# Performance work log

Measured on AMD Instinct MI355X. Metric: run time of the kernel, lower is better.

## Reference

```python
import jax, jax.numpy as jnp
import numpy as np

N = 50000      # nodes per graph (= num hyperedges, forced by the stack ops)
E = 800000     # incidence pairs per graph
L = 16         # max nodes per hyperedge (padded with index 0)
F_IN = 128     # in_channels
D1 = 256       # dim_1
D2 = D1 // 4   # conv2 out dim = FusionAttention in_size
H_ATT = 128    # FusionAttention hidden_size
EPS = 1e-15


def setup_inputs() -> dict:
    key = jax.random.key(0)
    ks = jax.random.split(key, 32)
    inp = {}
    for i in range(4):
        inp[f"x{i}"] = jax.random.normal(ks[i], (N, F_IN), jnp.float32)
        nidx = jax.random.randint(ks[4 + i], (E,), 0, N, dtype=jnp.int32)
        eidx = jax.random.randint(ks[8 + i], (E,), 0, N, dtype=jnp.int32)
        inp[f"ei{i}"] = jnp.stack([nidx, eidx])  # [2, E]
        hn = jax.random.randint(ks[12 + i], (N, L), 0, N + 1, dtype=jnp.int32)
        inp[f"hnode{i}"] = hn
        # hye_len = number of real (non-padding) entries per hyperedge
        inp[f"hlen{i}"] = jnp.sum(hn > 0, axis=1, keepdims=True).astype(jnp.float32)
    # shared Hgnn params (PyG HypergraphConv: lin without bias + separate bias)
    inp["W1"] = jax.random.normal(ks[16], (F_IN, D1), jnp.float32) / np.sqrt(F_IN).astype(np.float32)
    inp["b1"] = jnp.zeros((D1,), jnp.float32)
    inp["W2"] = jax.random.normal(ks[17], (D1, D2), jnp.float32) / np.sqrt(D1).astype(np.float32)
    inp["b2"] = jnp.zeros((D2,), jnp.float32)
    # two FusionAttention heads: Linear(D2,H_ATT)+Tanh, Linear(H_ATT,1,bias=False)
    for name, a, b in [("ac", 18, 19), ("am", 20, 21)]:
        inp[f"{name}_W1"] = jax.random.normal(ks[a], (D2, H_ATT), jnp.float32) / np.sqrt(D2).astype(np.float32)
        inp[f"{name}_b1"] = jnp.zeros((H_ATT,), jnp.float32)
        inp[f"{name}_W2"] = jax.random.normal(ks[b], (H_ATT, 1), jnp.float32) / np.sqrt(H_ATT).astype(np.float32)
    return inp


def _hconv(x, node_idx, edge_idx, W, b):
    """PyG HypergraphConv (heads=1, unit hyperedge weights):
    X' = D^-1 H B^-1 H^T (X W) + b, via two segment-sum passes."""
    x = x @ W  # [N, out]
    ones = jnp.ones(node_idx.shape, x.dtype)
    deg_n = jax.ops.segment_sum(ones, node_idx, num_segments=N)
    d_inv = jnp.where(deg_n > 0, 1.0 / deg_n, 0.0)
    deg_e = jax.ops.segment_sum(ones, edge_idx, num_segments=N)
    b_inv = jnp.where(deg_e > 0, 1.0 / deg_e, 0.0)
    # node -> hyperedge: m_e = B^-1[e] * sum_{v in e} x[v]
    efeat = b_inv[:, None] * jax.ops.segment_sum(x[node_idx], edge_idx, num_segments=N)
    # hyperedge -> node: out_v = D^-1[v] * sum_{e : v in e} m_e
    out = d_inv[:, None] * jax.ops.segment_sum(efeat[edge_idx], node_idx, num_segments=N)
    return out + b


def _hgnn(x, ei, W1, b1, W2, b2):
    x = jax.nn.relu(_hconv(x, ei[0], ei[1], W1, b1))
    return jax.nn.relu(_hconv(x, ei[0], ei[1], W2, b2))


def _hye_emb(node_emb, hlen, hnode):
    # prepend zero row so padding index 0 gathers zeros
    padded = jnp.concatenate([jnp.zeros((1, node_emb.shape[1]), node_emb.dtype), node_emb], axis=0)
    seq = padded[hnode]                    # [M, L, F]
    return jnp.sum(seq, axis=1) / (hlen + EPS)


def _fusion_attn(z, W1, b1, W2):
    # z: [N, 4, d]
    w = (jnp.tanh(z @ W1 + b1) @ W2).mean(0)      # [4, 1]
    beta = jax.nn.softmax(w, axis=0)              # [4, 1]
    return jnp.sum(beta * z, axis=1)              # [N, d]


def reference(x0, x1, x2, x3, ei0, ei1, ei2, ei3,
              hlen0, hlen1, hlen2, hlen3, hnode0, hnode1, hnode2, hnode3,
              W1, b1, W2, b2, ac_W1, ac_b1, ac_W2, am_W1, am_b1, am_W2):
    x1_cm = _hgnn(x0, ei0, W1, b1, W2, b2)
    x1_mc = _hgnn(x1, ei1, W1, b1, W2, b2)
    x1_cc = _hgnn(x2, ei2, W1, b1, W2, b2)
    x1_mm = _hgnn(x3, ei3, W1, b1, W2, b2)
    x2_cm = _hye_emb(x1_cm, hlen0, hnode0)
    x2_mc = _hye_emb(x1_mc, hlen1, hnode1)
    x2_cc = _hye_emb(x1_cc, hlen2, hnode2)
    x2_mm = _hye_emb(x1_mm, hlen3, hnode3)
    x_c = jnp.stack((x1_mc, x2_cm, x1_cc, x2_cc), axis=1)  # [N, 4, D2]
    x_m = jnp.stack((x1_cm, x2_mc, x1_mm, x2_mm), axis=1)
    h_c = _fusion_attn(x_c, ac_W1, ac_b1, ac_W2)
    h_m = _fusion_attn(x_m, am_W1, am_b1, am_W2)
    return (h_c, h_m)
```

## Files before the change

kernel.cpp:

```cpp
#include <hip/hip_runtime.h>
#include <hip/hip_bf16.h>

#define NF   128
#define DD1  256
#define DD2  64
#define HATT 128

static inline int cdiv(int a, int b) { return (a + b - 1) / b; }

__global__ __launch_bounds__(256) void count_rank(const int* __restrict__ nidx,
                                                  const int* __restrict__ eidx,
                                                  int* __restrict__ deg,
                                                  int* __restrict__ rank,
                                                  int N, int E) {
    int e = blockIdx.x * 256 + threadIdx.x;
    if (e < E) {
        const int vn = nidx[e], ve = eidx[e];
        const int rn = atomicAdd(&deg[vn], 1);
        const int re = atomicAdd(&deg[N + ve], 1);
        rank[e] = rn | (re << 16);
    }
}

__global__ __launch_bounds__(256) void scan_blocks(const int* __restrict__ in,
// ... 106 lines not shown
        a.rank[(size_t)g * a.E + e] = rn | (re << 16);
    }
}

__global__ __launch_bounds__(256) void build_fill_b(BuildB a) {
    const int g = blockIdx.y;
    const int shard = blockIdx.x & 7;
    const int chunk = blockIdx.x >> 3;
    const int lo = shard * a.shardSize;
    const int hi = lo + a.shardSize;
    const int base = chunk * 1024;
    const int* __restrict__ nidx = a.nidx[g];
    const int* __restrict__ eidx = a.eidx[g];
    const int* __restrict__ rank = a.rank + (size_t)g * a.E;
    const int* __restrict__ off  = a.off + (size_t)g * 2 * a.Nn;
#pragma unroll
    for (int i = 0; i < 4; i++) {
        const int e = base + i * 256 + threadIdx.x;
        if (e < a.E) {
            const int vn = nidx[e], ve = eidx[e];
            const int rk = rank[e];
            if (vn >= lo && vn < hi)
                a.srcidx[off[vn] + (rk & 0xffff)] = ve;
            if (ve >= lo && ve < hi)
                a.srcidx[off[a.Nn + ve] + (rk >> 16)] = vn;
        }
    }
}

__global__ __launch_bounds__(256) void gather_rows_128(const float* __restrict__ src,
                                                       const int* __restrict__ off,
                                                       const int* __restrict__ srcidx,
                                                       const float* __restrict__ scale,
                                                       float* __restrict__ dst, int Nn) {
    const int row = blockIdx.x * 16 + (threadIdx.x >> 4);
    if (row >= Nn) return;
    const int c = (threadIdx.x & 15) << 2;
    const int j0 = off[row], j1 = off[row + 1];
    float4 pa = make_float4(0.f, 0.f, 0.f, 0.f);
    float4 pb = make_float4(0.f, 0.f, 0.f, 0.f);
    float4 qa = make_float4(0.f, 0.f, 0.f, 0.f);
    float4 qb = make_float4(0.f, 0.f, 0.f, 0.f);
    int j = j0;
    for (; j + 3 < j1; j += 4) {
        const int s0 = srcidx[j + 0];
        const int s1 = srcidx[j + 1];
        const int s2 = srcidx[j + 2];
        const int s3 = srcidx[j + 3];
        const float4 v0a = *(const float4*)&src[(size_t)s0 * 128 + c];
        const float4 v0b = *(const float4*)&src[(size_t)s0 * 128 + c + 64];
        const float4 v1a = *(const float4*)&src[(size_t)s1 * 128 + c];
        const float4 v1b = *(const float4*)&src[(size_t)s1 * 128 + c + 64];
        const float4 v2a = *(const float4*)&src[(size_t)s2 * 128 + c];
        const float4 v2b = *(const float4*)&src[(size_t)s2 * 128 + c + 64];
        const float4 v3a = *(const float4*)&src[(size_t)s3 * 128 + c];
        const float4 v3b = *(const float4*)&src[(size_t)s3 * 128 + c + 64];
        pa.x += v0a.x + v1a.x; pa.y += v0a.y + v1a.y;
        pa.z += v0a.z + v1a.z; pa.w += v0a.w + v1a.w;
        qa.x += v2a.x + v3a.x; qa.y += v2a.y + v3a.y;
        qa.z += v2a.z + v3a.z; qa.w += v2a.w + v3a.w;
        pb.x += v0b.x + v1b.x; pb.y += v0b.y + v1b.y;
        pb.z += v0b.z + v1b.z; pb.w += v0b.w + v1b.w;
        qb.x += v2b.x + v3b.x; qb.y += v2b.y + v3b.y;
        qb.z += v2b.z + v3b.z; qb.w += v2b.w + v3b.w;
    }
    for (; j < j1; j++) {
        const int s0 = srcidx[j];
        const float4 va = *(const float4*)&src[(size_t)s0 * 128 + c];
        const float4 vb = *(const float4*)&src[(size_t)s0 * 128 + c + 64];
        pa.x += va.x; pa.y += va.y; pa.z += va.z; pa.w += va.w;
        pb.x += vb.x; pb.y += vb.y; pb.z += vb.z; pb.w += vb.w;
    }
    float4 aca = make_float4(pa.x + qa.x, pa.y + qa.y, pa.z + qa.z, pa.w + qa.w);
    float4 acb = make_float4(pb.x + qb.x, pb.y + qb.y, pb.z + qb.z, pb.w + qb.w);
    if (scale) {
        const float s = scale[row];
        aca.x *= s; aca.y *= s; aca.z *= s; aca.w *= s;
        acb.x *= s; acb.y *= s; acb.z *= s; acb.w *= s;
    }
    *(float4*)&dst[(size_t)row * 128 + c] = aca;
    *(float4*)&dst[(size_t)row * 128 + c + 64] = acb;
}

struct Gather128B {
    const float* src[4];
    float* dst;
    const int* off;
    const int* srcidx;
    const float* dinv;
    int passBase;
    int Nn;
};

__global__ __launch_bounds__(256) void gather128_b(Gather128B a) {
    const int gr = blockIdx.x * 16 + (threadIdx.x >> 4);
    if (gr >= 4 * a.Nn) return;
    const int g = gr / a.Nn;
    const int row = gr - g * a.Nn;
    const float* __restrict__ src = a.src[g];
    const int ob = g * 2 * a.Nn + a.passBase + row;
    const int c = (threadIdx.x & 15) << 2;
    const int j0 = a.off[ob], j1 = a.off[ob + 1];
    float4 pa = make_float4(0.f, 0.f, 0.f, 0.f);
    float4 pb = make_float4(0.f, 0.f, 0.f, 0.f);
    float4 qa = make_float4(0.f, 0.f, 0.f, 0.f);
    float4 qb = make_float4(0.f, 0.f, 0.f, 0.f);
    int j = j0;
    for (; j + 3 < j1; j += 4) {
        const int s0 = a.srcidx[j + 0];
        const int s1 = a.srcidx[j + 1];
        const int s2 = a.srcidx[j + 2];
        const int s3 = a.srcidx[j + 3];
        const float4 v0a = *(const float4*)&src[(size_t)s0 * 128 + c];
        const float4 v0b = *(const float4*)&src[(size_t)s0 * 128 + c + 64];
        const float4 v1a = *(const float4*)&src[(size_t)s1 * 128 + c];
        const float4 v1b = *(const float4*)&src[(size_t)s1 * 128 + c + 64];
        const float4 v2a = *(const float4*)&src[(size_t)s2 * 128 + c];
        const float4 v2b = *(const float4*)&src[(size_t)s2 * 128 + c + 64];
        const float4 v3a = *(const float4*)&src[(size_t)s3 * 128 + c];
        const float4 v3b = *(const float4*)&src[(size_t)s3 * 128 + c + 64];
        pa.x += v0a.x + v1a.x; pa.y += v0a.y + v1a.y;
        pa.z += v0a.z + v1a.z; pa.w += v0a.w + v1a.w;
        qa.x += v2a.x + v3a.x; qa.y += v2a.y + v3a.y;
        qa.z += v2a.z + v3a.z; qa.w += v2a.w + v3a.w;
        pb.x += v0b.x + v1b.x; pb.y += v0b.y + v1b.y;
        pb.z += v0b.z + v1b.z; pb.w += v0b.w + v1b.w;
        qb.x += v2b.x + v3b.x; qb.y += v2b.y + v3b.y;
        qb.z += v2b.z + v3b.z; qb.w += v2b.w + v3b.w;
    }
    for (; j < j1; j++) {
        const int s0 = a.srcidx[j];
        const float4 va = *(const float4*)&src[(size_t)s0 * 128 + c];
        const float4 vb = *(const float4*)&src[(size_t)s0 * 128 + c + 64];
        pa.x += va.x; pa.y += va.y; pa.z += va.z; pa.w += va.w;
        pb.x += vb.x; pb.y += vb.y; pb.z += vb.z; pb.w += vb.w;
    }
    float4 aca = make_float4(pa.x + qa.x, pa.y + qa.y, pa.z + qa.z, pa.w + qa.w);
    float4 acb = make_float4(pb.x + qb.x, pb.y + qb.y, pb.z + qb.z, pb.w + qb.w);
    if (a.dinv) {
        const float s = a.dinv[ob];
        aca.x *= s; aca.y *= s; aca.z *= s; aca.w *= s;
        acb.x *= s; acb.y *= s; acb.z *= s; acb.w *= s;
    }
    *(float4*)&a.dst[(size_t)gr * 128 + c] = aca;
    *(float4*)&a.dst[(size_t)gr * 128 + c + 64] = acb;
}

__global__ __launch_bounds__(256) void gather_rows_64(const float* __restrict__ src,
                                                      const int* __restrict__ off,
                                                      const int* __restrict__ srcidx,
                                                      const float* __restrict__ scale,
                                                      const float* __restrict__ post_bias,
                                                      float* __restrict__ dst, int Nn) {
    const int row = blockIdx.x * 32 + (threadIdx.x >> 3);
    if (row >= Nn) return;
    const int c = (threadIdx.x & 7) << 2;
    const int j0 = off[row], j1 = off[row + 1];
    float4 pa = make_float4(0.f, 0.f, 0.f, 0.f);
    float4 pb = make_float4(0.f, 0.f, 0.f, 0.f);
    float4 qa = make_float4(0.f, 0.f, 0.f, 0.f);
    float4 qb = make_float4(0.f, 0.f, 0.f, 0.f);
    int j = j0;
    for (; j + 3 < j1; j += 4) {
        const int s0 = srcidx[j + 0];
        const int s1 = srcidx[j + 1];
        const int s2 = srcidx[j + 2];
        const int s3 = srcidx[j + 3];
        const float4 v0a = *(const float4*)&src[(size_t)s0 * 64 + c];
        const float4 v0b = *(const float4*)&src[(size_t)s0 * 64 + c + 32];
        const float4 v1a = *(const float4*)&src[(size_t)s1 * 64 + c];
        const float4 v1b = *(const float4*)&src[(size_t)s1 * 64 + c + 32];
        const float4 v2a = *(const float4*)&src[(size_t)s2 * 64 + c];
        const float4 v2b = *(const float4*)&src[(size_t)s2 * 64 + c + 32];
        const float4 v3a = *(const float4*)&src[(size_t)s3 * 64 + c];
        const float4 v3b = *(const float4*)&src[(size_t)s3 * 64 + c + 32];
        pa.x += v0a.x + v1a.x; pa.y += v0a.y + v1a.y;
        pa.z += v0a.z + v1a.z; pa.w += v0a.w + v1a.w;
        qa.x += v2a.x + v3a.x; qa.y += v2a.y + v3a.y;
        qa.z += v2a.z + v3a.z; qa.w += v2a.w + v3a.w;
        pb.x += v0b.x + v1b.x; pb.y += v0b.y + v1b.y;
        pb.z += v0b.z + v1b.z; pb.w += v0b.w + v1b.w;
        qb.x += v2b.x + v3b.x; qb.y += v2b.y + v3b.y;
        qb.z += v2b.z + v3b.z; qb.w += v2b.w + v3b.w;
// ... 91 lines not shown
        aca.x = fmaxf(aca.x + a.post_bias[c + 0], 0.f);
        aca.y = fmaxf(aca.y + a.post_bias[c + 1], 0.f);
        aca.z = fmaxf(aca.z + a.post_bias[c + 2], 0.f);
        aca.w = fmaxf(aca.w + a.post_bias[c + 3], 0.f);
        acb.x = fmaxf(acb.x + a.post_bias[c + 32], 0.f);
        acb.y = fmaxf(acb.y + a.post_bias[c + 33], 0.f);
        acb.z = fmaxf(acb.z + a.post_bias[c + 34], 0.f);
        acb.w = fmaxf(acb.w + a.post_bias[c + 35], 0.f);
    }
    *(float4*)&a.dst[(size_t)gr * 64 + c] = aca;
    *(float4*)&a.dst[(size_t)gr * 64 + c + 32] = acb;
}

__global__ __launch_bounds__(256) void gemm1_f32(const float* __restrict__ A,
                                                 const float* __restrict__ B,
                                                 float* __restrict__ C, int M,
                                                 const float* __restrict__ dinv,
                                                 const float* __restrict__ bias) {
    __shared__ float As[32][132];
    __shared__ float Bs[32][128];
    const int tid = threadIdx.x;
    const int m0 = blockIdx.y * 128;
    const int bn = blockIdx.x * 128;
    const int rq = (tid >> 4) << 2;
    const int cq = (tid & 15) << 2;

    float acc[8][8] = {{0.f}};

    for (int k0 = 0; k0 < 128; k0 += 32) {
#pragma unroll
        for (int i = 0; i < 4; i++) {
            const int f = tid + 256 * i;
            const int r = f >> 3;
            const int q = (f & 7) << 2;
            const int grow = m0 + r;
            float4 v = make_float4(0.f, 0.f, 0.f, 0.f);
            if (grow < M) v = *(const float4*)&A[(size_t)grow * 128 + k0 + q];
            As[q + 0][r] = v.x;
            As[q + 1][r] = v.y;
            As[q + 2][r] = v.z;
            As[q + 3][r] = v.w;
        }
#pragma unroll
        for (int i = 0; i < 4; i++) {
            const int f = tid + 256 * i;
            const int r = f >> 5;
            const int c4 = (f & 31) << 2;
            *(float4*)&Bs[r][c4] = *(const float4*)&B[(size_t)(k0 + r) * 256 + bn + c4];
        }
        __syncthreads();
#pragma unroll
        for (int k = 0; k < 32; k++) {
            float av[8], bv[8];
            *(float4*)&av[0] = *(const float4*)&As[k][rq];
            *(float4*)&av[4] = *(const float4*)&As[k][rq + 64];
            *(float4*)&bv[0] = *(const float4*)&Bs[k][cq];
            *(float4*)&bv[4] = *(const float4*)&Bs[k][cq + 64];
#pragma unroll
            for (int r = 0; r < 8; r++)
#pragma unroll
                for (int c = 0; c < 8; c++)
                    acc[r][c] = fmaf(av[r], bv[c], acc[r][c]);
        }
        __syncthreads();
    }
#pragma unroll
    for (int r = 0; r < 8; r++) {
        const int grow = m0 + rq + (r & 3) + ((r >> 2) << 6);
        if (grow < M) {
            const float s = dinv[grow];
            float o[8];
#pragma unroll
            for (int c = 0; c < 4; c++)
                o[c] = fmaxf(fmaf(acc[r][c], s, bias[bn + cq + c]), 0.f);
#pragma unroll
            for (int c = 4; c < 8; c++)
                o[c] = fmaxf(fmaf(acc[r][c], s, bias[bn + 64 + cq + (c - 4)]), 0.f);
            *(float4*)&C[(size_t)grow * 256 + bn + cq] = *(float4*)&o[0];
            *(float4*)&C[(size_t)grow * 256 + bn + 64 + cq] = *(float4*)&o[4];
        }
    }
}

struct Gemm1B {
    const float* A;
    const float* B;
    float* C[4];
    const float* dinv;
    const float* bias;
    int Nn;
};

__global__ __launch_bounds__(256) void gemm1_b(Gemm1B a) {
    __shared__ float As[32][132];
    __shared__ float Bs[32][128];
    const int M = 4 * a.Nn;
    const int tid = threadIdx.x;
    const int m0 = blockIdx.y * 128;
    const int bn = blockIdx.x * 128;
    const int rq = (tid >> 4) << 2;
    const int cq = (tid & 15) << 2;

    float acc[8][8] = {{0.f}};

    for (int k0 = 0; k0 < 128; k0 += 32) {
#pragma unroll
        for (int i = 0; i < 4; i++) {
            const int f = tid + 256 * i;
            const int r = f >> 3;
            const int q = (f & 7) << 2;
            const int grow = m0 + r;
            float4 v = make_float4(0.f, 0.f, 0.f, 0.f);
            if (grow < M) v = *(const float4*)&a.A[(size_t)grow * 128 + k0 + q];
            As[q + 0][r] = v.x;
            As[q + 1][r] = v.y;
            As[q + 2][r] = v.z;
            As[q + 3][r] = v.w;
        }
#pragma unroll
        for (int i = 0; i < 4; i++) {
            const int f = tid + 256 * i;
            const int r = f >> 5;
            const int c4 = (f & 31) << 2;
            *(float4*)&Bs[r][c4] = *(const float4*)&a.B[(size_t)(k0 + r) * 256 + bn + c4];
        }
        __syncthreads();
#pragma unroll
        for (int k = 0; k < 32; k++) {
            float av[8], bv[8];
            *(float4*)&av[0] = *(const float4*)&As[k][rq];
            *(float4*)&av[4] = *(const float4*)&As[k][rq + 64];
            *(float4*)&bv[0] = *(const float4*)&Bs[k][cq];
            *(float4*)&bv[4] = *(const float4*)&Bs[k][cq + 64];
#pragma unroll
            for (int r = 0; r < 8; r++)
#pragma unroll
                for (int c = 0; c < 8; c++)
                    acc[r][c] = fmaf(av[r], bv[c], acc[r][c]);
        }
        __syncthreads();
    }
#pragma unroll
    for (int r = 0; r < 8; r++) {
        const int grow = m0 + rq + (r & 3) + ((r >> 2) << 6);
        if (grow < M) {
            const int g = grow / a.Nn;
            const int lr = grow - g * a.Nn;
            const float s = a.dinv[(size_t)g * 2 * a.Nn + lr];
            float* Cg = a.C[g] + (size_t)lr * 256;
            float o[8];
#pragma unroll
            for (int c = 0; c < 4; c++)
                o[c] = fmaxf(fmaf(acc[r][c], s, a.bias[bn + cq + c]), 0.f);
#pragma unroll
            for (int c = 4; c < 8; c++)
                o[c] = fmaxf(fmaf(acc[r][c], s, a.bias[bn + 64 + cq + (c - 4)]), 0.f);
            *(float4*)&Cg[bn + cq] = *(float4*)&o[0];
            *(float4*)&Cg[bn + 64 + cq] = *(float4*)&o[4];
        }
    }
}

__global__ __launch_bounds__(256) void gemm2_f32(const float* __restrict__ A,
                                                 const float* __restrict__ B,
                                                 float* __restrict__ C, int M) {
    __shared__ float As[32][132];
    __shared__ float Bs[32][64];
    const int tid = threadIdx.x;
    const int m0 = blockIdx.y * 128;
    const int tr = (tid >> 3) << 2;
    const int tc = (tid & 7) << 3;

    float acc[4][8] = {{0.f}};

    for (int k0 = 0; k0 < 256; k0 += 32) {
#pragma unroll
        for (int i = 0; i < 4; i++) {
            const int f = tid + 256 * i;
            const int r = f >> 3;
            const int q = (f & 7) << 2;
            const int grow = m0 + r;
            float4 v = make_float4(0.f, 0.f, 0.f, 0.f);
            if (grow < M) v = *(const float4*)&A[(size_t)grow * 256 + k0 + q];
            As[q + 0][r] = v.x;
            As[q + 1][r] = v.y;
            As[q + 2][r] = v.z;
            As[q + 3][r] = v.w;
        }
#pragma unroll
        for (int i = 0; i < 2; i++) {
            const int f = tid + 256 * i;
            const int r = f >> 4;
            const int c4 = (f & 15) << 2;
            *(float4*)&Bs[r][c4] = *(const float4*)&B[(size_t)(k0 + r) * 64 + c4];
        }
        __syncthreads();
#pragma unroll
        for (int k = 0; k < 32; k++) {
            float av[4], bv[8];
            *(float4*)&av[0] = *(const float4*)&As[k][tr];
            *(float4*)&bv[0] = *(const float4*)&Bs[k][tc];
            *(float4*)&bv[4] = *(const float4*)&Bs[k][tc + 4];
#pragma unroll
            for (int r = 0; r < 4; r++)
#pragma unroll
                for (int c = 0; c < 8; c++)
                    acc[r][c] = fmaf(av[r], bv[c], acc[r][c]);
        }
        __syncthreads();
    }
#pragma unroll
    for (int r = 0; r < 4; r++) {
        const int grow = m0 + tr + r;
        if (grow < M) {
            *(float4*)&C[(size_t)grow * 64 + tc] =
                make_float4(acc[r][0], acc[r][1], acc[r][2], acc[r][3]);
            *(float4*)&C[(size_t)grow * 64 + tc + 4] =
                make_float4(acc[r][4], acc[r][5], acc[r][6], acc[r][7]);
        }
    }
}

struct Gemm2B {
    const float* A[4];
    const float* B;
    float* C;
    int Nn;
};

__global__ __launch_bounds__(256) void gemm2_b(Gemm2B a) {
    __shared__ float As[32][132];
    __shared__ float Bs[32][64];
    const int M = 4 * a.Nn;
    const int tid = threadIdx.x;
    const int m0 = blockIdx.y * 128;
    const int tr = (tid >> 3) << 2;
    const int tc = (tid & 7) << 3;

    float acc[4][8] = {{0.f}};

    for (int k0 = 0; k0 < 256; k0 += 32) {
#pragma unroll
        for (int i = 0; i < 4; i++) {
            const int f = tid + 256 * i;
            const int r = f >> 3;
            const int q = (f & 7) << 2;
            const int grow = m0 + r;
            float4 v = make_float4(0.f, 0.f, 0.f, 0.f);
            if (grow < M) {
                const int g = grow / a.Nn;
                const int lr = grow - g * a.Nn;
                v = *(const float4*)&a.A[g][(size_t)lr * 256 + k0 + q];
            }
            As[q + 0][r] = v.x;
            As[q + 1][r] = v.y;
            As[q + 2][r] = v.z;
            As[q + 3][r] = v.w;
        }
#pragma unroll
        for (int i = 0; i < 2; i++) {
            const int f = tid + 256 * i;
            const int r = f >> 4;
            const int c4 = (f & 15) << 2;
            *(float4*)&Bs[r][c4] = *(const float4*)&a.B[(size_t)(k0 + r) * 64 + c4];
        }
        __syncthreads();
#pragma unroll
        for (int k = 0; k < 32; k++) {
            float av[4], bv[8];
            *(float4*)&av[0] = *(const float4*)&As[k][tr];
            *(float4*)&bv[0] = *(const float4*)&Bs[k][tc];
            *(float4*)&bv[4] = *(const float4*)&Bs[k][tc + 4];
#pragma unroll
            for (int r = 0; r < 4; r++)
#pragma unroll
                for (int c = 0; c < 8; c++)
                    acc[r][c] = fmaf(av[r], bv[c], acc[r][c]);
        }
        __syncthreads();
    }
#pragma unroll
    for (int r = 0; r < 4; r++) {
        const int grow = m0 + tr + r;
        if (grow < M) {
            *(float4*)&a.C[(size_t)grow * 64 + tc] =
                make_float4(acc[r][0], acc[r][1], acc[r][2], acc[r][3]);
            *(float4*)&a.C[(size_t)grow * 64 + tc + 4] =
                make_float4(acc[r][4], acc[r][5], acc[r][6], acc[r][7]);
        }
    }
}

__global__ __launch_bounds__(256) void hye_emb_kernel(const float* __restrict__ emb,
                                                      const int* __restrict__ hnode,
                                                      const float* __restrict__ hlen,
                                                      float* __restrict__ out, int Nn) {
    const int r = blockIdx.x * 16 + (threadIdx.x >> 4);
    const int c = (threadIdx.x & 15) << 2;
    if (r >= Nn) return;
    const int4* hp4 = (const int4*)&hnode[(size_t)r * 16];
    const int4 w0 = hp4[0], w1 = hp4[1], w2 = hp4[2], w3 = hp4[3];
    int idx[16] = {w0.x, w0.y, w0.z, w0.w, w1.x, w1.y, w1.z, w1.w,
                   w2.x, w2.y, w2.z, w2.w, w3.x, w3.y, w3.z, w3.w};
    float4 a0 = make_float4(0.f, 0.f, 0.f, 0.f);
    float4 a1 = make_float4(0.f, 0.f, 0.f, 0.f);
    float4 a2 = make_float4(0.f, 0.f, 0.f, 0.f);
    float4 a3 = make_float4(0.f, 0.f, 0.f, 0.f);
#pragma unroll
    for (int l = 0; l < 16; l += 4) {
        if (idx[l + 0] > 0) {
            const float4 v = *(const float4*)&emb[(size_t)(idx[l + 0] - 1) * 64 + c];
            a0.x += v.x; a0.y += v.y; a0.z += v.z; a0.w += v.w;
        }
        if (idx[l + 1] > 0) {
            const float4 v = *(const float4*)&emb[(size_t)(idx[l + 1] - 1) * 64 + c];
            a1.x += v.x; a1.y += v.y; a1.z += v.z; a1.w += v.w;
        }
        if (idx[l + 2] > 0) {
            const float4 v = *(const float4*)&emb[(size_t)(idx[l + 2] - 1) * 64 + c];
            a2.x += v.x; a2.y += v.y; a2.z += v.z; a2.w += v.w;
        }
        if (idx[l + 3] > 0) {
            const float4 v = *(const float4*)&emb[(size_t)(idx[l + 3] - 1) * 64 + c];
            a3.x += v.x; a3.y += v.y; a3.z += v.z; a3.w += v.w;
        }
    }
    const float inv = 1.0f / (hlen[r] + 1e-15f);
    float4 acc;
    acc.x = (a0.x + a1.x + a2.x + a3.x) * inv;
    acc.y = (a0.y + a1.y + a2.y + a3.y) * inv;
    acc.z = (a0.z + a1.z + a2.z + a3.z) * inv;
    acc.w = (a0.w + a1.w + a2.w + a3.w) * inv;
    *(float4*)&out[(size_t)r * 64 + c] = acc;
}

struct HyeB {
    const float* emb;
    const int* hnode[4];
    const float* hlen[4];
    float* out;
    int Nn;
};

__global__ __launch_bounds__(256) void hye_b(HyeB a) {
    const int gr = blockIdx.x * 16 + (threadIdx.x >> 4);
    const int c = (threadIdx.x & 15) << 2;
    if (gr >= 4 * a.Nn) return;
    const int g = gr / a.Nn;
    const int lr = gr - g * a.Nn;
    const float* __restrict__ emb = a.emb + (size_t)g * a.Nn * 64;
    const int4* hp4 = (const int4*)&a.hnode[g][(size_t)lr * 16];
    const int4 w0 = hp4[0], w1 = hp4[1], w2 = hp4[2], w3 = hp4[3];
    int idx[16] = {w0.x, w0.y, w0.z, w0.w, w1.x, w1.y, w1.z, w1.w,
                   w2.x, w2.y, w2.z, w2.w, w3.x, w3.y, w3.z, w3.w};
    float4 a0 = make_float4(0.f, 0.f, 0.f, 0.f);
    float4 a1 = make_float4(0.f, 0.f, 0.f, 0.f);
    float4 a2 = make_float4(0.f, 0.f, 0.f, 0.f);
    float4 a3 = make_float4(0.f, 0.f, 0.f, 0.f);
#pragma unroll
    for (int l = 0; l < 16; l += 4) {
        if (idx[l + 0] > 0) {
            const float4 v = *(const float4*)&emb[(size_t)(idx[l + 0] - 1) * 64 + c];
            a0.x += v.x; a0.y += v.y; a0.z += v.z; a0.w += v.w;
        }
        if (idx[l + 1] > 0) {
            const float4 v = *(const float4*)&emb[(size_t)(idx[l + 1] - 1) * 64 + c];
            a1.x += v.x; a1.y += v.y; a1.z += v.z; a1.w += v.w;
        }
        if (idx[l + 2] > 0) {
            const float4 v = *(const float4*)&emb[(size_t)(idx[l + 2] - 1) * 64 + c];
            a2.x += v.x; a2.y += v.y; a2.z += v.z; a2.w += v.w;
        }
// ... 85 lines not shown
        if (m0 + mq + r < a.Nn) {
#pragma unroll
            for (int c = 0; c < 8; c++) {
                float s = acc[r][c] + b1v[c];
                s = fminf(fmaxf(s, -15.f), 15.f);
                const float t = __expf(2.f * s);
                local += (1.f - 2.f / (t + 1.f)) * w2v[c];
            }
        }
    }
#pragma unroll
    for (int off = 32; off >= 1; off >>= 1) local += __shfl_down(local, off, 64);
    if ((tid & 63) == 0) red[tid >> 6] = local;
    __syncthreads();
    if (tid == 0) atomicAdd(&a.accw[gy], red[0] + red[1] + red[2] + red[3]);
}

__global__ void softmax_beta(const float* __restrict__ acc, float* __restrict__ beta,
                             float invN) {
    const int t = threadIdx.x;
    if (t < 2) {
        const float* a = acc + 4 * t;
        float* b = beta + 4 * t;
        float w[4], m = -1e30f;
#pragma unroll
        for (int i = 0; i < 4; i++) { w[i] = a[i] * invN; m = fmaxf(m, w[i]); }
        float s = 0.f;
#pragma unroll
        for (int i = 0; i < 4; i++) { w[i] = expf(w[i] - m); s += w[i]; }
#pragma unroll
        for (int i = 0; i < 4; i++) b[i] = w[i] / s;
    }
}

__global__ __launch_bounds__(256) void weighted_sum(const float* __restrict__ z0,
                                                    const float* __restrict__ z1,
                                                    const float* __restrict__ z2,
                                                    const float* __restrict__ z3,
                                                    const float* __restrict__ beta,
                                                    float* __restrict__ out, int Nn) {
    const int t = blockIdx.x * 256 + threadIdx.x;
    if (t >= Nn * 16) return;
    const float b0 = beta[0], b1 = beta[1], b2 = beta[2], b3 = beta[3];
    const float4 v0 = *(const float4*)&z0[(size_t)t * 4];
    const float4 v1 = *(const float4*)&z1[(size_t)t * 4];
    const float4 v2 = *(const float4*)&z2[(size_t)t * 4];
    const float4 v3 = *(const float4*)&z3[(size_t)t * 4];
    float4 o;
    o.x = b0 * v0.x + b1 * v1.x + b2 * v2.x + b3 * v3.x;
    o.y = b0 * v0.y + b1 * v1.y + b2 * v2.y + b3 * v3.y;
    o.z = b0 * v0.z + b1 * v1.z + b2 * v2.z + b3 * v3.z;
    o.w = b0 * v0.w + b1 * v1.w + b2 * v2.w + b3 * v3.w;
    *(float4*)&out[(size_t)t * 4] = o;
}

extern "C" void kernel_launch(void* const* d_in, const int* in_sizes, int n_in,
                              void* d_out, int out_size, void* d_ws, size_t ws_size,
                              hipStream_t stream) {
    const int Nn = in_sizes[0] / NF;
    const int E  = in_sizes[1] / 2;
    const int N2 = 2 * Nn;

    const float* x[4];
    const int*   ei[4];
    const int*   hnode[4];
    const float* hlen[4];
    for (int g = 0; g < 4; g++) {
        x[g]     = (const float*)d_in[4 * g + 0];
        ei[g]    = (const int*)d_in[4 * g + 1];
        hnode[g] = (const int*)d_in[4 * g + 2];
        hlen[g]  = (const float*)d_in[4 * g + 3];
    }
    const float* W1   = (const float*)d_in[16];
    const float* b1   = (const float*)d_in[17];
    const float* W2   = (const float*)d_in[18];
    const float* b2   = (const float*)d_in[19];
    const float* acW1 = (const float*)d_in[20];
    const float* acb1 = (const float*)d_in[21];
    const float* acW2 = (const float*)d_in[22];
    const float* amW1 = (const float*)d_in[23];
    const float* amb1 = (const float*)d_in[24];
    const float* amW2 = (const float*)d_in[25];

    const size_t fB1   = (size_t)4 * Nn * 128;
    const size_t fB2   = (size_t)4 * Nn * 128;
    const size_t fH2   = (size_t)4 * Nn * 64;
    const size_t fHE   = (size_t)4 * Nn * 64;
    const size_t fDinv = (size_t)4 * N2;
    const size_t fcnt  = fB1 + fB2 + fH2 + fHE + fDinv + 16;
    const size_t icnt  = (size_t)4 * N2 + ((size_t)4 * N2 + 4) + 512 +
                         (size_t)4 * E + (size_t)8 * E;
    const size_t need  = (fcnt + icnt) * sizeof(float) + 1024;

    if (need <= ws_size) {
        float* ws = (float*)d_ws;
        size_t o = 0;
        float* B1    = ws + o; o += fB1;
        float* B2    = ws + o; o += fB2;
        float* h2b   = ws + o; o += fH2;
        float* hembb = ws + o; o += fHE;
        float* dinv  = ws + o; o += fDinv;
        float* accw  = ws + o; o += 8;
        float* beta  = ws + o; o += 8;
        int* iws = (int*)(ws + o);
        size_t io = 0;
        int* deg      = iws + io; io += (size_t)4 * N2;
        int* off      = iws + io; io += (size_t)4 * N2 + 4;
        int* partials = iws + io; io += 512;
        int* rank     = iws + io; io += (size_t)4 * E;
        int* srcidx   = iws + io; io += (size_t)8 * E;

        float* C1p[4] = { B1, B1 + (size_t)Nn * 256, h2b, hembb };
        float* Dbuf = B2;
        float* E1   = B2 + (size_t)Nn * 256;

        const int n8  = 4 * N2;
        const int nScanBlocks = cdiv(n8, 1024);

        BuildB bb;
        for (int g = 0; g < 4; g++) { bb.nidx[g] = ei[g]; bb.eidx[g] = ei[g] + E; }
        bb.deg = deg; bb.rank = rank; bb.off = off; bb.srcidx = srcidx;
        bb.Nn = Nn; bb.E = E; bb.shardSize = cdiv(Nn, 8);

        hipMemsetAsync(deg, 0, (size_t)n8 * sizeof(int), stream);
        count_rank_b<<<dim3(cdiv(E, 256), 4), 256, 0, stream>>>(bb);
        scan_blocks<<<nScanBlocks, 256, 0, stream>>>(deg, off, partials, n8);
        scan_partials<<<1, 512, 0, stream>>>(partials, nScanBlocks);
        scan_add<<<cdiv(n8, 256), 256, 0, stream>>>(off, partials, n8, 2 * 4 * E);
        build_fill_b<<<dim3(8 * cdiv(E, 1024), 4), 256, 0, stream>>>(bb);
        invert_deg_int<<<cdiv(n8, 256), 256, 0, stream>>>(deg, dinv, n8);

        Gather128B g1;
        for (int g = 0; g < 4; g++) g1.src[g] = x[g];
        g1.dst = B1; g1.off = off; g1.srcidx = srcidx;
        g1.dinv = dinv; g1.passBase = Nn; g1.Nn = Nn;
        gather128_b<<<cdiv(4 * Nn, 16), 256, 0, stream>>>(g1);

        Gather128B g2;
        for (int g = 0; g < 4; g++) g2.src[g] = B1 + (size_t)g * Nn * 128;
        g2.dst = B2; g2.off = off; g2.srcidx = srcidx;
        g2.dinv = nullptr; g2.passBase = 0; g2.Nn = Nn;
        gather128_b<<<cdiv(4 * Nn, 16), 256, 0, stream>>>(g2);

        Gemm1B gm1;
        gm1.A = B2; gm1.B = W1;
        for (int g = 0; g < 4; g++) gm1.C[g] = C1p[g];
        gm1.dinv = dinv; gm1.bias = b1; gm1.Nn = Nn;
        gemm1_b<<<dim3(2, cdiv(4 * Nn, 128)), 256, 0, stream>>>(gm1);

        Gemm2B gm2;
        for (int g = 0; g < 4; g++) gm2.A[g] = C1p[g];
        gm2.B = W2; gm2.C = Dbuf; gm2.Nn = Nn;
        gemm2_b<<<dim3(1, cdiv(4 * Nn, 128)), 256, 0, stream>>>(gm2);

        Gather64B g3;
        for (int g = 0; g < 4; g++) g3.src[g] = Dbuf + (size_t)g * Nn * 64;
        g3.dst = E1; g3.off = off; g3.srcidx = srcidx;
        g3.dinv = dinv; g3.post_bias = nullptr; g3.passBase = Nn; g3.Nn = Nn;
        gather64_b<<<cdiv(4 * Nn, 32), 256, 0, stream>>>(g3);

        Gather64B g4;
        for (int g = 0; g < 4; g++) g4.src[g] = E1 + (size_t)g * Nn * 64;
        g4.dst = h2b; g4.off = off; g4.srcidx = srcidx;
        g4.dinv = dinv; g4.post_bias = b2; g4.passBase = 0; g4.Nn = Nn;
        gather64_b<<<cdiv(4 * Nn, 32), 256, 0, stream>>>(g4);

        HyeB hb;
        hb.emb = h2b;
        for (int g = 0; g < 4; g++) { hb.hnode[g] = hnode[g]; hb.hlen[g] = hlen[g]; }
        hb.out = hembb; hb.Nn = Nn;
        hye_b<<<cdiv(4 * Nn, 16), 256, 0, stream>>>(hb);

        const size_t st = (size_t)Nn * 64;
        hipMemsetAsync(accw, 0, 8 * sizeof(float), stream);
        AttnArgs aa;
        aa.z[0] = h2b + 1 * st; aa.z[1] = hembb + 0 * st;
        aa.z[2] = h2b + 2 * st; aa.z[3] = hembb + 2 * st;
        aa.z[4] = h2b + 0 * st; aa.z[5] = hembb + 1 * st;
        aa.z[6] = h2b + 3 * st; aa.z[7] = hembb + 3 * st;
        aa.W1c = acW1; aa.b1c = acb1; aa.W2c = acW2;
        aa.W1m = amW1; aa.b1m = amb1; aa.W2m = amW2;
        aa.accw = accw; aa.Nn = Nn;
        attn_gemm<<<dim3(cdiv(Nn, 64), 8), 256, 0, stream>>>(aa);
        softmax_beta<<<1, 64, 0, stream>>>(accw, beta, 1.0f / (float)Nn);

        float* out = (float*)d_out;
        weighted_sum<<<cdiv(Nn * 16, 256), 256, 0, stream>>>(
            aa.z[0], aa.z[1], aa.z[2], aa.z[3], beta + 0, out, Nn);
        weighted_sum<<<cdiv(Nn * 16, 256), 256, 0, stream>>>(
            aa.z[4], aa.z[5], aa.z[6], aa.z[7], beta + 4, out + (size_t)Nn * DD2, Nn);
        return;
    }

    float* ws = (float*)d_ws;
    size_t o = 0;
    float* bufA = ws + o; o += (size_t)Nn * DD1;
    float* bufB = ws + o; o += (size_t)Nn * DD1;
    float* dinv = ws + o; o += N2;
    float* h2[4];
    float* hemb[4];
    for (int g = 0; g < 4; g++) { h2[g]   = ws + o; o += (size_t)Nn * DD2; }
    for (int g = 0; g < 4; g++) { hemb[g] = ws + o; o += (size_t)Nn * DD2; }
    float* accw = ws + o; o += 8;
    float* beta = ws + o; o += 8;
    int* iws = (int*)(ws + o);
    size_t io = 0;
    int* deg_i    = iws + io; io += N2;
    int* off      = iws + io; io += N2 + 1;
    int* partials = iws + io; io += 512;
    int* rank     = iws + io; io += E;
    int* srcidx   = iws + io; io += (size_t)2 * E;

    const int nScanBlocks = cdiv(N2, 1024);
    const int shardSize = cdiv(Nn, 8);

    for (int g = 0; g < 4; g++) {
        const int* nidx = ei[g];
        const int* eidx = ei[g] + E;
        const int* off_n = off;
        const int* off_e = off + Nn;
        const float* d_inv = dinv;
        const float* b_inv = dinv + Nn;

        hipMemsetAsync(deg_i, 0, (size_t)N2 * sizeof(int), stream);
        count_rank<<<cdiv(E, 256), 256, 0, stream>>>(nidx, eidx, deg_i, rank, Nn, E);
        scan_blocks<<<nScanBlocks, 256, 0, stream>>>(deg_i, off, partials, N2);
        scan_partials<<<1, 512, 0, stream>>>(partials, nScanBlocks);
        scan_add<<<cdiv(N2, 256), 256, 0, stream>>>(off, partials, N2, 2 * E);
        build_fill<<<8 * cdiv(E, 1024), 256, 0, stream>>>(nidx, eidx, rank, off,
                                                          srcidx, Nn, E, shardSize);
        invert_deg_int<<<cdiv(N2, 256), 256, 0, stream>>>(deg_i, dinv, N2);

        gather_rows_128<<<cdiv(Nn, 16), 256, 0, stream>>>(x[g], off_e, srcidx, b_inv, bufB, Nn);
        gather_rows_128<<<cdiv(Nn, 16), 256, 0, stream>>>(bufB, off_n, srcidx, nullptr, bufA, Nn);
        gemm1_f32<<<dim3(2, cdiv(Nn, 128)), 256, 0, stream>>>(bufA, W1, bufB, Nn, d_inv, b1);

        gemm2_f32<<<dim3(1, cdiv(Nn, 128)), 256, 0, stream>>>(bufB, W2, bufA, Nn);
        gather_rows_64<<<cdiv(Nn, 32), 256, 0, stream>>>(bufA, off_e, srcidx, b_inv,
                                                         nullptr, bufB, Nn);
        gather_rows_64<<<cdiv(Nn, 32), 256, 0, stream>>>(bufB, off_n, srcidx, d_inv,
                                                         b2, h2[g], Nn);

        hye_emb_kernel<<<cdiv(Nn, 16), 256, 0, stream>>>(h2[g], hnode[g], hlen[g], hemb[g], Nn);
    }

    hipMemsetAsync(accw, 0, 8 * sizeof(float), stream);
    AttnArgs aa;
    aa.z[0] = h2[1]; aa.z[1] = hemb[0]; aa.z[2] = h2[2]; aa.z[3] = hemb[2];
    aa.z[4] = h2[0]; aa.z[5] = hemb[1]; aa.z[6] = h2[3]; aa.z[7] = hemb[3];
// ... 13 lines not shown
```

Measured before the change: 1.875 ms.

## Fuse two hypergraph GEMMs into one kernel and shrink workspace via buffer aliasing

Merges the 128->256 and 256->64 GEMMs into one kernel that keeps the 256-wide intermediate in shared memory, so that intermediate never goes to global memory. The 128-wide gathers now run in two halves of two graphs each, and deg/rank/intermediate buffers are aliased onto one region to cut the workspace footprint and improve cache residency. The fused GEMM uses small 32-row tiles with a scalar second-stage inner loop, which may lower compute efficiency. The split gathers add kernel launches.

```diff
diff --git a/kernel.cpp b/kernel.cpp
--- a/kernel.cpp
+++ b/kernel.cpp
@@ -212,23 +212,24 @@
     *(float4*)&dst[(size_t)row * 128 + c + 64] = acb;
 }
 
-struct Gather128B {
-    const float* src[4];
+struct Gather128H {
+    const float* src[2];
     float* dst;
     const int* off;
     const int* srcidx;
     const float* dinv;
+    int gbase;
     int passBase;
     int Nn;
 };
 
-__global__ __launch_bounds__(256) void gather128_b(Gather128B a) {
+__global__ __launch_bounds__(256) void gather128_h(Gather128H a) {
     const int gr = blockIdx.x * 16 + (threadIdx.x >> 4);
-    if (gr >= 4 * a.Nn) return;
-    const int g = gr / a.Nn;
-    const int row = gr - g * a.Nn;
-    const float* __restrict__ src = a.src[g];
-    const int ob = g * 2 * a.Nn + a.passBase + row;
+    if (gr >= 2 * a.Nn) return;
+    const int gl = gr / a.Nn;
+    const int row = gr - gl * a.Nn;
+    const float* __restrict__ src = a.src[gl];
+    const int ob = (a.gbase + gl) * 2 * a.Nn + a.passBase + row;
     const int c = (threadIdx.x & 15) << 2;
     const int j0 = a.off[ob], j1 = a.off[ob + 1];
     float4 pa = make_float4(0.f, 0.f, 0.f, 0.f);
@@ -486,85 +487,6 @@
     }
 }
 
-struct Gemm1B {
-    const float* A;
-    const float* B;
-    float* C[4];
-    const float* dinv;
-    const float* bias;
-    int Nn;
-};
-
-__global__ __launch_bounds__(256) void gemm1_b(Gemm1B a) {
-    __shared__ float As[32][132];
-    __shared__ float Bs[32][128];
-    const int M = 4 * a.Nn;
-    const int tid = threadIdx.x;
-    const int m0 = blockIdx.y * 128;
-    const int bn = blockIdx.x * 128;
-    const int rq = (tid >> 4) << 2;
-    const int cq = (tid & 15) << 2;
-
-    float acc[8][8] = {{0.f}};
-
-    for (int k0 = 0; k0 < 128; k0 += 32) {
-#pragma unroll
-        for (int i = 0; i < 4; i++) {
-            const int f = tid + 256 * i;
-            const int r = f >> 3;
-            const int q = (f & 7) << 2;
-            const int grow = m0 + r;
-            float4 v = make_float4(0.f, 0.f, 0.f, 0.f);
-            if (grow < M) v = *(const float4*)&a.A[(size_t)grow * 128 + k0 + q];
-            As[q + 0][r] = v.x;
-            As[q + 1][r] = v.y;
-            As[q + 2][r] = v.z;
-            As[q + 3][r] = v.w;
-        }
-#pragma unroll
-        for (int i = 0; i < 4; i++) {
-            const int f = tid + 256 * i;
-            const int r = f >> 5;
-            const int c4 = (f & 31) << 2;
-            *(float4*)&Bs[r][c4] = *(const float4*)&a.B[(size_t)(k0 + r) * 256 + bn + c4];
-        }
-        __syncthreads();
-#pragma unroll
-        for (int k = 0; k < 32; k++) {
-            float av[8], bv[8];
-            *(float4*)&av[0] = *(const float4*)&As[k][rq];
-            *(float4*)&av[4] = *(const float4*)&As[k][rq + 64];
-            *(float4*)&bv[0] = *(const float4*)&Bs[k][cq];
-            *(float4*)&bv[4] = *(const float4*)&Bs[k][cq + 64];
-#pragma unroll
-            for (int r = 0; r < 8; r++)
-#pragma unroll
-                for (int c = 0; c < 8; c++)
-                    acc[r][c] = fmaf(av[r], bv[c], acc[r][c]);
-        }
-        __syncthreads();
-    }
-#pragma unroll
-    for (int r = 0; r < 8; r++) {
-        const int grow = m0 + rq + (r & 3) + ((r >> 2) << 6);
-        if (grow < M) {
-            const int g = grow / a.Nn;
-            const int lr = grow - g * a.Nn;
-            const float s = a.dinv[(size_t)g * 2 * a.Nn + lr];
-            float* Cg = a.C[g] + (size_t)lr * 256;
-            float o[8];
-#pragma unroll
-            for (int c = 0; c < 4; c++)
-                o[c] = fmaxf(fmaf(acc[r][c], s, a.bias[bn + cq + c]), 0.f);
-#pragma unroll
-            for (int c = 4; c < 8; c++)
-                o[c] = fmaxf(fmaf(acc[r][c], s, a.bias[bn + 64 + cq + (c - 4)]), 0.f);
-            *(float4*)&Cg[bn + cq] = *(float4*)&o[0];
-            *(float4*)&Cg[bn + 64 + cq] = *(float4*)&o[4];
-        }
-    }
-}
-
 __global__ __launch_bounds__(256) void gemm2_f32(const float* __restrict__ A,
                                                  const float* __restrict__ B,
                                                  float* __restrict__ C, int M) {
@@ -625,56 +547,59 @@
     }
 }
 
-struct Gemm2B {
-    const float* A[4];
-    const float* B;
-    float* C;
+struct Gemm12B {
+    const float* A;
+    const float* W1;
+    const float* W2;
+    const float* b1;
+    const float* dinv;
+    float* D;
     int Nn;
 };
 
-__global__ __launch_bounds__(256) void gemm2_b(Gemm2B a) {
-    __shared__ float As[32][132];
-    __shared__ float Bs[32][64];
-    const int M = 4 * a.Nn;
+#define TS_LD 33
+
+__global__ __launch_bounds__(256) void gemm12_b(Gemm12B a) {
+    __shared__ float smem[9472];
+    float* As  = smem;
+    float* Bs  = smem + 1152;
+    float* Ts  = smem;
+    float* W2s = smem + 8448;
+
+    const int M4 = 4 * a.Nn;
     const int tid = threadIdx.x;
-    const int m0 = blockIdx.y * 128;
-    const int tr = (tid >> 3) << 2;
-    const int tc = (tid & 7) << 3;
+    const int m0 = blockIdx.x * 32;
+    const int rq = (tid >> 5) << 2;
+    const int cq = (tid & 31) << 2;
 
     float acc[4][8] = {{0.f}};
 
-    for (int k0 = 0; k0 < 256; k0 += 32) {
-#pragma unroll
-        for (int i = 0; i < 4; i++) {
-            const int f = tid + 256 * i;
-            const int r = f >> 3;
-            const int q = (f & 7) << 2;
+    for (int k0 = 0; k0 < 128; k0 += 32) {
+        {
+            const int r = tid >> 3;
+            const int q = (tid & 7) << 2;
             const int grow = m0 + r;
             float4 v = make_float4(0.f, 0.f, 0.f, 0.f);
-            if (grow < M) {
-                const int g = grow / a.Nn;
-                const int lr = grow - g * a.Nn;
-                v = *(const float4*)&a.A[g][(size_t)lr * 256 + k0 + q];
-            }
-            As[q + 0][r] = v.x;
-            As[q + 1][r] = v.y;
-            As[q + 2][r] = v.z;
-            As[q + 3][r] = v.w;
-        }
-#pragma unroll
-        for (int i = 0; i < 2; i++) {
+            if (grow < M4) v = *(const float4*)&a.A[(size_t)grow * 128 + k0 + q];
+            As[(q + 0) * 36 + r] = v.x;
+            As[(q + 1) * 36 + r] = v.y;
+            As[(q + 2) * 36 + r] = v.z;
+            As[(q + 3) * 36 + r] = v.w;
+        }
+#pragma unroll
+        for (int i = 0; i < 8; i++) {
             const int f = tid + 256 * i;
-            const int r = f >> 4;
-            const int c4 = (f & 15) << 2;
-            *(float4*)&Bs[r][c4] = *(const float4*)&a.B[(size_t)(k0 + r) * 64 + c4];
+            const int r = f >> 6;
+            const int c4 = (f & 63) << 2;
+            *(float4*)&Bs[r * 256 + c4] = *(const float4*)&a.W1[(size_t)(k0 + r) * 256 + c4];
         }
         __syncthreads();
 #pragma unroll
         for (int k = 0; k < 32; k++) {
             float av[4], bv[8];
-            *(float4*)&av[0] = *(const float4*)&As[k][tr];
-            *(float4*)&bv[0] = *(const float4*)&Bs[k][tc];
-            *(float4*)&bv[4] = *(const float4*)&Bs[k][tc + 4];
+            *(float4*)&av[0] = *(const float4*)&As[k * 36 + rq];
+            *(float4*)&bv[0] = *(const float4*)&Bs[k * 256 + cq];
+            *(float4*)&bv[4] = *(const float4*)&Bs[k * 256 + cq + 128];
 #pragma unroll
             for (int r = 0; r < 4; r++)
 #pragma unroll
@@ -683,15 +608,64 @@
         }
         __syncthreads();
     }
+
+    {
+        float b1lo[4], b1hi[4], s[4];
+#pragma unroll
+        for (int j = 0; j < 4; j++) {
+            b1lo[j] = a.b1[cq + j];
+            b1hi[j] = a.b1[cq + 128 + j];
+        }
+#pragma unroll
+        for (int r = 0; r < 4; r++) {
+            const int gr = m0 + rq + r;
+            float sv = 0.f;
+            if (gr < M4) {
+                const int g = gr / a.Nn;
+                const int lr = gr - g * a.Nn;
+                sv = a.dinv[(size_t)g * 2 * a.Nn + lr];
+            }
+            s[r] = sv;
+        }
+#pragma unroll
+        for (int r = 0; r < 4; r++)
+#pragma unroll
+            for (int j = 0; j < 4; j++) {
+                Ts[(cq + j) * TS_LD + rq + r] =
+                    fmaxf(fmaf(acc[r][j], s[r], b1lo[j]), 0.f);
+                Ts[(cq + 128 + j) * TS_LD + rq + r] =
+                    fmaxf(fmaf(acc[r][4 + j], s[r], b1hi[j]), 0.f);
+            }
+    }
+
+    const int c2 = (tid & 31) << 1;
+    float d0[4] = {0.f, 0.f, 0.f, 0.f};
+    float d1[4] = {0.f, 0.f, 0.f, 0.f};
+    for (int kk = 0; kk < 256; kk += 16) {
+        __syncthreads();
+        {
+            const int r = tid >> 4;
+            const int c4 = (tid & 15) << 2;
+            *(float4*)&W2s[r * 64 + c4] = *(const float4*)&a.W2[(size_t)(kk + r) * 64 + c4];
+        }
+        __syncthreads();
+#pragma unroll
+        for (int k = 0; k < 16; k++) {
+            const float* tr = &Ts[(kk + k) * TS_LD + rq];
+            const float t0 = tr[0], t1 = tr[1], t2 = tr[2], t3 = tr[3];
+            const float w0 = W2s[k * 64 + c2];
+            const float w1 = W2s[k * 64 + c2 + 1];
+            d0[0] = fmaf(t0, w0, d0[0]); d1[0] = fmaf(t0, w1, d1[0]);
+            d0[1] = fmaf(t1, w0, d0[1]); d1[1] = fmaf(t1, w1, d1[1]);
+            d0[2] = fmaf(t2, w0, d0[2]); d1[2] = fmaf(t2, w1, d1[2]);
+            d0[3] = fmaf(t3, w0, d0[3]); d1[3] = fmaf(t3, w1, d1[3]);
+        }
+    }
 #pragma unroll
     for (int r = 0; r < 4; r++) {
-        const int grow = m0 + tr + r;
-        if (grow < M) {
-            *(float4*)&a.C[(size_t)grow * 64 + tc] =
-                make_float4(acc[r][0], acc[r][1], acc[r][2], acc[r][3]);
-            *(float4*)&a.C[(size_t)grow * 64 + tc + 4] =
-                make_float4(acc[r][4], acc[r][5], acc[r][6], acc[r][7]);
-        }
+        const int gr = m0 + rq + r;
+        if (gr < M4)
+            *(float2*)&a.D[(size_t)gr * 64 + c2] = make_float2(d0[r], d1[r]);
     }
 }
 
@@ -943,39 +917,32 @@
     const float* amb1 = (const float*)d_in[24];
     const float* amW2 = (const float*)d_in[25];
 
-    const size_t fB1   = (size_t)4 * Nn * 128;
-    const size_t fB2   = (size_t)4 * Nn * 128;
-    const size_t fH2   = (size_t)4 * Nn * 64;
-    const size_t fHE   = (size_t)4 * Nn * 64;
+    const size_t fRA   = (size_t)4 * Nn * 64;
+    const size_t fRB   = (size_t)4 * Nn * 128;
     const size_t fDinv = (size_t)4 * N2;
-    const size_t fcnt  = fB1 + fB2 + fH2 + fHE + fDinv + 16;
-    const size_t icnt  = (size_t)4 * N2 + ((size_t)4 * N2 + 4) + 512 +
-                         (size_t)4 * E + (size_t)8 * E;
-    const size_t need  = (fcnt + icnt) * sizeof(float) + 1024;
-
-    if (need <= ws_size) {
+    const size_t fcnt  = fRA + fRB + fDinv + 16;
+    const size_t icnt  = ((size_t)4 * N2 + 4) + 512 + (size_t)8 * E;
+    const size_t need  = (fcnt + icnt) * sizeof(float) + 256;
+    const bool raFitsInts = fRA * sizeof(float) >=
+                            ((size_t)4 * N2 + (size_t)4 * E) * sizeof(int);
+
+    if (need <= ws_size && raFitsInts) {
         float* ws = (float*)d_ws;
         size_t o = 0;
-        float* B1    = ws + o; o += fB1;
-        float* B2    = ws + o; o += fB2;
-        float* h2b   = ws + o; o += fH2;
-        float* hembb = ws + o; o += fHE;
-        float* dinv  = ws + o; o += fDinv;
-        float* accw  = ws + o; o += 8;
-        float* beta  = ws + o; o += 8;
+        float* RA   = ws + o; o += fRA;
+        float* RB   = ws + o; o += fRB;
+        float* dinv = ws + o; o += fDinv;
+        float* accw = ws + o; o += 8;
+        float* beta = ws + o; o += 8;
         int* iws = (int*)(ws + o);
         size_t io = 0;
-        int* deg      = iws + io; io += (size_t)4 * N2;
         int* off      = iws + io; io += (size_t)4 * N2 + 4;
         int* partials = iws + io; io += 512;
-        int* rank     = iws + io; io += (size_t)4 * E;
         int* srcidx   = iws + io; io += (size_t)8 * E;
-
-        float* C1p[4] = { B1, B1 + (size_t)Nn * 256, h2b, hembb };
-        float* Dbuf = B2;
-        float* E1   = B2 + (size_t)Nn * 256;
-
-        const int n8  = 4 * N2;
+        int* deg  = (int*)RA;
+        int* rank = deg + (size_t)4 * N2;
+
+        const int n8 = 4 * N2;
         const int nScanBlocks = cdiv(n8, 1024);
 
         BuildB bb;
@@ -991,29 +958,31 @@
         build_fill_b<<<dim3(8 * cdiv(E, 1024), 4), 256, 0, stream>>>(bb);
         invert_deg_int<<<cdiv(n8, 256), 256, 0, stream>>>(deg, dinv, n8);
 
-        Gather128B g1;
-        for (int g = 0; g < 4; g++) g1.src[g] = x[g];
-        g1.dst = B1; g1.off = off; g1.srcidx = srcidx;
-        g1.dinv = dinv; g1.passBase = Nn; g1.Nn = Nn;
-        gather128_b<<<cdiv(4 * Nn, 16), 256, 0, stream>>>(g1);
-
-        Gather128B g2;
-        for (int g = 0; g < 4; g++) g2.src[g] = B1 + (size_t)g * Nn * 128;
-        g2.dst = B2; g2.off = off; g2.srcidx = srcidx;
-        g2.dinv = nullptr; g2.passBase = 0; g2.Nn = Nn;
-        gather128_b<<<cdiv(4 * Nn, 16), 256, 0, stream>>>(g2);
-
-        Gemm1B gm1;
-        gm1.A = B2; gm1.B = W1;
-        for (int g = 0; g < 4; g++) gm1.C[g] = C1p[g];
-        gm1.dinv = dinv; gm1.bias = b1; gm1.Nn = Nn;
-        gemm1_b<<<dim3(2, cdiv(4 * Nn, 128)), 256, 0, stream>>>(gm1);
-
-        Gemm2B gm2;
-        for (int g = 0; g < 4; g++) gm2.A[g] = C1p[g];
-        gm2.B = W2; gm2.C = Dbuf; gm2.Nn = Nn;
-        gemm2_b<<<dim3(1, cdiv(4 * Nn, 128)), 256, 0, stream>>>(gm2);
-
+        const int gh = cdiv(2 * Nn, 16);
+        for (int h = 0; h < 2; h++) {
+            const int gb = 2 * h;
+            Gather128H p1;
+            p1.src[0] = x[gb]; p1.src[1] = x[gb + 1];
+            p1.dst = RA; p1.off = off; p1.srcidx = srcidx;
+            p1.dinv = dinv; p1.gbase = gb; p1.passBase = Nn; p1.Nn = Nn;
+            gather128_h<<<gh, 256, 0, stream>>>(p1);
+
+            Gather128H p2;
+            p2.src[0] = RA; p2.src[1] = RA + (size_t)Nn * 128;
+            p2.dst = RB + (size_t)gb * Nn * 128;
+            p2.off = off; p2.srcidx = srcidx;
+            p2.dinv = nullptr; p2.gbase = gb; p2.passBase = 0; p2.Nn = Nn;
+            gather128_h<<<gh, 256, 0, stream>>>(p2);
+        }
+
+        float* Dbuf = RA;
+        Gemm12B gm;
+        gm.A = RB; gm.W1 = W1; gm.W2 = W2; gm.b1 = b1;
+        gm.dinv = dinv; gm.D = Dbuf; gm.Nn = Nn;
+        gemm12_b<<<cdiv(4 * Nn, 32), 256, 0, stream>>>(gm);
+
+        float* E1  = RB + (size_t)4 * Nn * 64;
+        float* h2b = RB;
         Gather64B g3;
         for (int g = 0; g < 4; g++) g3.src[g] = Dbuf + (size_t)g * Nn * 64;
         g3.dst = E1; g3.off = off; g3.srcidx = srcidx;
@@ -1026,6 +995,7 @@
         g4.dinv = dinv; g4.post_bias = b2; g4.passBase = 0; g4.Nn = Nn;
         gather64_b<<<cdiv(4 * Nn, 32), 256, 0, stream>>>(g4);
 
+        float* hembb = RA;
         HyeB hb;
         hb.emb = h2b;
         for (int g = 0; g < 4; g++) { hb.hnode[g] = hnode[g]; hb.hlen[g] = hlen[g]; }
```

Measured after the change: 1.706 ms. 9.0% less time.
